# Kernel optimization log

Hardware: AMD Instinct MI355X
Metric: run time of the kernel (lower is better)

## Reference

```python
import jax, jax.numpy as jnp
import numpy as np

N = 43
H = N // 2  # 21


def _mk(key, i, o):
    kw, kb = jax.random.split(key)
    bound = 1.0 / np.sqrt(i)
    W = jax.random.uniform(kw, (i, o), jnp.float32, -bound, bound)
    b = jax.random.uniform(kb, (o,), jnp.float32, -bound, bound)
    return W, b


def setup_inputs() -> dict:
    key = jax.random.key(0)
    keys = jax.random.split(key, 11)
    x = jax.random.normal(keys[0], (1048576, N), jnp.float32)
    dims = [(N, N), (N, N), (N, N), (N, N), (N, H),  # encoder
            (H, N), (N, N), (N, N), (N, N), (N, N)]  # decoder
    out = {"x": x}
    for li, (i, o) in enumerate(dims):
        W, b = _mk(keys[li + 1], i, o)
        out[f"W{li}"] = W
        out[f"b{li}"] = b
    return out


def reference(x, W0, b0, W1, b1, W2, b2, W3, b3, W4, b4,
              W5, b5, W6, b6, W7, b7, W8, b8, W9, b9):
    Ws = [W0, W1, W2, W3, W4, W5, W6, W7, W8, W9]
    bs = [b0, b1, b2, b3, b4, b5, b6, b7, b8, b9]
    h = x
    for li in range(10):
        h = h @ Ws[li] + bs[li]
        # tanh after every layer except encoder bottleneck (4) and final (9)
        if li not in (4, 9):
            h = jnp.tanh(h)
    return h
```

## Files before the change

kernel.cpp:

```cpp
#include <hip/hip_runtime.h>


typedef _Float16 f16x8 __attribute__((ext_vector_type(8)));
typedef float f32x4 __attribute__((ext_vector_type(4)));

#define TPB 512
#define NBLK 256
#define ITERS 16
#define NROWS 1048576
#define NCOL 43
#define WSTRIDE 72
#define WSLOT (48 * WSTRIDE)
#define W_BYTES (10 * WSLOT * 2)
#define XBUF_BYTES 6144
#define X_BASE W_BYTES
#define HBUF_BYTES (32 * WSTRIDE * 2)
#define H_BASE (X_BASE + 8 * XBUF_BYTES)
#define SMEM_BYTES (H_BASE + 8 * HBUF_BYTES)

__device__ __forceinline__ float fast_tanh(float x) {
  float t = __builtin_amdgcn_exp2f(x * 2.8853900817779268f);
  float r = __builtin_amdgcn_rcpf(t + 1.0f);
  return __builtin_fmaf(-2.0f, r, 1.0f);
}

__device__ __forceinline__ void gload_lds16(const void* g, void* l) {
  __builtin_amdgcn_global_load_lds(
      (const __attribute__((address_space(1))) void*)g,
      (__attribute__((address_space(3))) void*)l, 16, 0, 0);
}

__device__ __forceinline__ void issue_dma(const float* x, const char* xlim,
                                          float* xb, size_t rowbase, int lane) {
  const char* base = (const char*)x + rowbase * (size_t)(NCOL * 4);
#pragma unroll
  for (int c = 0; c < 6; ++c) {
    const char* src = base + c * 1024 + lane * 16;
    src = (src > xlim) ? xlim : src;
    gload_lds16(src, (char*)xb + c * 1024);
  }
}

__device__ __forceinline__ void store_h4(_Float16* dst, float v0, float v1,
                                         float v2, float v3) {
  union { _Float16 h[4]; uint2 u; } p;
  p.h[0] = (_Float16)v0; p.h[1] = (_Float16)v1;
  p.h[2] = (_Float16)v2; p.h[3] = (_Float16)v3;
  *(uint2*)dst = p.u;
}

template <int NT, int KC, bool DOTANH, int NLOUT>
__device__ __forceinline__ void mid_layer(const _Float16* __restrict__ Wl,
                                          _Float16* Hw, int g, int lr) {
  f16x8 Bv[2][KC];
#pragma unroll
  for (int s = 0; s < 2; ++s)
#pragma unroll
    for (int c = 0; c < KC; ++c)
      Bv[s][c] = *(const f16x8*)(Hw + (16 * s + lr) * WSTRIDE + 8 * g + 32 * c);

  f32x4 acc[NT][2];
#pragma unroll
  for (int t = 0; t < NT; ++t)
#pragma unroll
    for (int s = 0; s < 2; ++s) acc[t][s] = f32x4{0.f, 0.f, 0.f, 0.f};

#pragma unroll
  for (int c = 0; c < KC; ++c)
#pragma unroll
    for (int t = 0; t < NT; ++t) {
      f16x8 A = *(const f16x8*)(Wl + (16 * t + lr) * WSTRIDE + 8 * g + 32 * c);
#pragma unroll
      for (int s = 0; s < 2; ++s)
        acc[t][s] = __builtin_amdgcn_mfma_f32_16x16x32_f16(A, Bv[s][c],
                                                           acc[t][s], 0, 0, 0);
    }

#pragma unroll
  for (int t = 0; t < NT; ++t)
#pragma unroll
    for (int s = 0; s < 2; ++s) {
      float v[4];
#pragma unroll
      for (int r = 0; r < 4; ++r) {
        int col = 16 * t + 4 * g + r;
        float u = acc[t][s][r];
        if (DOTANH) u = fast_tanh(u);
        v[r] = (col < NLOUT) ? u : ((col == NLOUT) ? 1.0f : 0.0f);
      }
      store_h4(Hw + (16 * s + lr) * WSTRIDE + 16 * t + 4 * g,
               v[0], v[1], v[2], v[3]);
    }
}

extern "C" __global__ void __launch_bounds__(TPB, 2)
ae_kernel(const float* __restrict__ x,
          const float* __restrict__ W0, const float* __restrict__ B0,
          const float* __restrict__ W1, const float* __restrict__ B1,
          const float* __restrict__ W2, const float* __restrict__ B2,
          const float* __restrict__ W3, const float* __restrict__ B3,
          const float* __restrict__ W4, const float* __restrict__ B4,
          const float* __restrict__ W5, const float* __restrict__ B5,
          const float* __restrict__ W6, const float* __restrict__ B6,
          const float* __restrict__ W7, const float* __restrict__ B7,
          const float* __restrict__ W8, const float* __restrict__ B8,
          const float* __restrict__ W9, const float* __restrict__ B9,
          float* __restrict__ out) {
  extern __shared__ char smem[];
  _Float16* lw = (_Float16*)smem;

  const int tid = threadIdx.x;
  const int wave = tid >> 6;
  const int lane = tid & 63;
  const int g = lane >> 4;
  const int lr = lane & 15;

  {
    const float* Wp[10] = {W0, W1, W2, W3, W4, W5, W6, W7, W8, W9};
    const float* Bp[10] = {B0, B1, B2, B3, B4, B5, B6, B7, B8, B9};
    const int KLs[10] = {43, 43, 43, 43, 43, 21, 43, 43, 43, 43};
    const int NLs[10] = {43, 43, 43, 43, 21, 43, 43, 43, 43, 43};
#pragma unroll
    for (int L = 0; L < 10; ++L) {
      const float* Wl = Wp[L];
      const float* Bl = Bp[L];
      const int KL = KLs[L], NL = NLs[L];
      for (int idx = tid; idx < 48 * 64; idx += TPB) {
        int n = idx >> 6, k = idx & 63;
        float v = 0.0f;
        if (n < NL) {
          if (k < KL) v = Wl[k * NL + n];
          else if (k == KL && L != 0) v = Bl[n];
        }
        lw[L * WSLOT + n * WSTRIDE + k] = (_Float16)v;
      }
    }
  }

  float* xb = (float*)(smem + X_BASE + wave * XBUF_BYTES);
  _Float16* Hw = (_Float16*)(smem + H_BASE + wave * HBUF_BYTES);

  {
    unsigned* h32 = (unsigned*)Hw;
#pragma unroll
    for (int i = 0; i < 18; ++i) h32[lane + 64 * i] = 0;
  }

  float b0v[12];
#pragma unroll
  for (int t = 0; t < 3; ++t)
#pragma unroll
    for (int r = 0; r < 4; ++r) {
      int n = 16 * t + 4 * g + r;
      b0v[t * 4 + r] = (n < NCOL) ? B0[n] : 0.0f;
    }

  __syncthreads();

  const char* xlim = (const char*)x + (size_t)NROWS * NCOL * 4 - 16;
  const size_t blockrow = (size_t)blockIdx.x * (ITERS * 256);

  issue_dma(x, xlim, xb, blockrow + (size_t)(wave * 32), lane);

#pragma unroll 1
  for (int it = 0; it < ITERS; ++it) {
    const size_t row0 = blockrow + (size_t)it * 256 + (size_t)(wave * 32);
    asm volatile("s_waitcnt vmcnt(0)" ::: "memory");

    f16x8 Bv[2][2];
#pragma unroll
    for (int s = 0; s < 2; ++s)
#pragma unroll
      for (int c = 0; c < 2; ++c) {
        const float* xr = xb + (16 * s + lr) * NCOL + 8 * g + 32 * c;
        f16x8 v;
#pragma unroll
        for (int j = 0; j < 8; ++j) v[j] = (_Float16)xr[j];
        Bv[s][c] = v;
      }
    asm volatile("s_waitcnt lgkmcnt(0)" ::: "memory");
    if (it < ITERS - 1)
      issue_dma(x, xlim, xb, row0 + 256, lane);

    f32x4 acc[3][2];
#pragma unroll
    for (int t = 0; t < 3; ++t)
#pragma unroll
      for (int s = 0; s < 2; ++s) acc[t][s] = f32x4{0.f, 0.f, 0.f, 0.f};
#pragma unroll
    for (int c = 0; c < 2; ++c)
#pragma unroll
      for (int t = 0; t < 3; ++t) {
        f16x8 A = *(const f16x8*)(lw + (16 * t + lr) * WSTRIDE + 8 * g + 32 * c);
#pragma unroll
        for (int s = 0; s < 2; ++s)
          acc[t][s] = __builtin_amdgcn_mfma_f32_16x16x32_f16(A, Bv[s][c],
                                                             acc[t][s], 0, 0, 0);
      }
#pragma unroll
    for (int t = 0; t < 3; ++t)
#pragma unroll
      for (int s = 0; s < 2; ++s) {
        float v[4];
#pragma unroll
        for (int r = 0; r < 4; ++r) {
          int col = 16 * t + 4 * g + r;
          float u = fast_tanh(acc[t][s][r] + b0v[t * 4 + r]);
          v[r] = (col < NCOL) ? u : ((col == NCOL) ? 1.0f : 0.0f);
        }
        store_h4(Hw + (16 * s + lr) * WSTRIDE + 16 * t + 4 * g,
                 v[0], v[1], v[2], v[3]);
      }

    mid_layer<3, 2, true, 43>(lw + 1 * WSLOT, Hw, g, lr);
    mid_layer<3, 2, true, 43>(lw + 2 * WSLOT, Hw, g, lr);
    mid_layer<3, 2, true, 43>(lw + 3 * WSLOT, Hw, g, lr);
    mid_layer<2, 2, false, 21>(lw + 4 * WSLOT, Hw, g, lr);
    mid_layer<3, 1, true, 43>(lw + 5 * WSLOT, Hw, g, lr);
    mid_layer<3, 2, true, 43>(lw + 6 * WSLOT, Hw, g, lr);
    mid_layer<3, 2, true, 43>(lw + 7 * WSLOT, Hw, g, lr);
    mid_layer<3, 2, true, 43>(lw + 8 * WSLOT, Hw, g, lr);

    {
      f16x8 B9[2][2];
#pragma unroll
      for (int s = 0; s < 2; ++s)
#pragma unroll
        for (int c = 0; c < 2; ++c)
          B9[s][c] = *(const f16x8*)(Hw + (16 * s + lr) * WSTRIDE + 8 * g + 32 * c);
      f32x4 a9[3][2];
#pragma unroll
      for (int t = 0; t < 3; ++t)
#pragma unroll
        for (int s = 0; s < 2; ++s) a9[t][s] = f32x4{0.f, 0.f, 0.f, 0.f};
#pragma unroll
      for (int c = 0; c < 2; ++c)
#pragma unroll
        for (int t = 0; t < 3; ++t) {
          f16x8 A = *(const f16x8*)(lw + 9 * WSLOT + (16 * t + lr) * WSTRIDE +
                                    8 * g + 32 * c);
#pragma unroll
          for (int s = 0; s < 2; ++s)
            a9[t][s] = __builtin_amdgcn_mfma_f32_16x16x32_f16(A, B9[s][c],
                                                              a9[t][s], 0, 0, 0);
        }
#pragma unroll
      for (int t = 0; t < 3; ++t)
#pragma unroll
        for (int s = 0; s < 2; ++s)
#pragma unroll
          for (int r = 0; r < 4; ++r) {
            int col = 16 * t + 4 * g + r;
            if (col < NCOL)
              out[(row0 + (size_t)(16 * s + lr)) * NCOL + col] = a9[t][s][r];
          }
    }
  }
}

extern "C" void kernel_launch(void* const* d_in, const int* in_sizes, int n_in,
                              void* d_out, int out_size, void* d_ws,
                              size_t ws_size, hipStream_t stream) {
  const float* x = (const float*)d_in[0];
  const float* W[10];
  const float* B[10];
  for (int i = 0; i < 10; ++i) {
    W[i] = (const float*)d_in[1 + 2 * i];
    B[i] = (const float*)d_in[2 + 2 * i];
  }
  hipFuncSetAttribute(reinterpret_cast<const void*>(ae_kernel),
                      hipFuncAttributeMaxDynamicSharedMemorySize, SMEM_BYTES);
  ae_kernel<<<dim3(NBLK), dim3(TPB), SMEM_BYTES, stream>>>(
      x, W[0], B[0], W[1], B[1], W[2], B[2], W[3], B[3], W[4], B[4],
      W[5], B[5], W[6], B[6], W[7], B[7], W[8], B[8], W[9], B[9],
      (float*)d_out);
}
```

Before: 169.0 us.

## Load x directly into registers with prefetch, drop LDS DMA staging, double block size

Removes the global-to-LDS DMA staging buffer for the input rows. Each lane now reads its x values straight into registers and prefetches the next iteration's rows during compute. Out-of-range columns are masked with a packed multiply. The block grows to 1024 threads (16 waves) with half the iterations, and conversions to half precision use packed round-toward-zero instructions. This cuts LDS traffic and wait barriers, but the scalar 4-byte global loads are uncoalesced, register pressure goes up, and the kernel is limited to one block per CU.

```diff
diff --git a/kernel.cpp b/kernel.cpp
--- a/kernel.cpp
+++ b/kernel.cpp
@@ -1,22 +1,24 @@
 #include <hip/hip_runtime.h>
 
 
+typedef __fp16 pk16x2 __attribute__((ext_vector_type(2)));
 typedef _Float16 f16x8 __attribute__((ext_vector_type(8)));
 typedef float f32x4 __attribute__((ext_vector_type(4)));
 
-#define TPB 512
+#define TPB 1024
 #define NBLK 256
-#define ITERS 16
+#define ITERS 8
 #define NROWS 1048576
 #define NCOL 43
+#define ROWB 172u
+#define XBYTES (NROWS * (size_t)ROWB)
 #define WSTRIDE 72
 #define WSLOT (48 * WSTRIDE)
 #define W_BYTES (10 * WSLOT * 2)
-#define XBUF_BYTES 6144
-#define X_BASE W_BYTES
-#define HBUF_BYTES (32 * WSTRIDE * 2)
-#define H_BASE (X_BASE + 8 * XBUF_BYTES)
-#define SMEM_BYTES (H_BASE + 8 * HBUF_BYTES)
+#define HBUF_HW (32 * WSTRIDE)
+#define HBUF_BYTES (HBUF_HW * 2)
+#define H_BASE W_BYTES
+#define SMEM_BYTES (H_BASE + 16 * HBUF_BYTES)
 
 __device__ __forceinline__ float fast_tanh(float x) {
   float t = __builtin_amdgcn_exp2f(x * 2.8853900817779268f);
@@ -24,28 +26,11 @@
   return __builtin_fmaf(-2.0f, r, 1.0f);
 }
 
-__device__ __forceinline__ void gload_lds16(const void* g, void* l) {
-  __builtin_amdgcn_global_load_lds(
-      (const __attribute__((address_space(1))) void*)g,
-      (__attribute__((address_space(3))) void*)l, 16, 0, 0);
-}
-
-__device__ __forceinline__ void issue_dma(const float* x, const char* xlim,
-                                          float* xb, size_t rowbase, int lane) {
-  const char* base = (const char*)x + rowbase * (size_t)(NCOL * 4);
-#pragma unroll
-  for (int c = 0; c < 6; ++c) {
-    const char* src = base + c * 1024 + lane * 16;
-    src = (src > xlim) ? xlim : src;
-    gload_lds16(src, (char*)xb + c * 1024);
-  }
-}
-
 __device__ __forceinline__ void store_h4(_Float16* dst, float v0, float v1,
                                          float v2, float v3) {
-  union { _Float16 h[4]; uint2 u; } p;
-  p.h[0] = (_Float16)v0; p.h[1] = (_Float16)v1;
-  p.h[2] = (_Float16)v2; p.h[3] = (_Float16)v3;
+  union { pk16x2 h[2]; uint2 u; } p;
+  p.h[0] = __builtin_amdgcn_cvt_pkrtz(v0, v1);
+  p.h[1] = __builtin_amdgcn_cvt_pkrtz(v2, v3);
   *(uint2*)dst = p.u;
 }
 
@@ -93,7 +78,7 @@
     }
 }
 
-extern "C" __global__ void __launch_bounds__(TPB, 2)
+extern "C" __global__ void __launch_bounds__(TPB, 1)
 ae_kernel(const float* __restrict__ x,
           const float* __restrict__ W0, const float* __restrict__ B0,
           const float* __restrict__ W1, const float* __restrict__ B1,
@@ -137,7 +122,6 @@
     }
   }
 
-  float* xb = (float*)(smem + X_BASE + wave * XBUF_BYTES);
   _Float16* Hw = (_Float16*)(smem + H_BASE + wave * HBUF_BYTES);
 
   {
@@ -155,32 +139,65 @@
       b0v[t * 4 + r] = (n < NCOL) ? B0[n] : 0.0f;
     }
 
+  pk16x2 m1[4];
+#pragma unroll
+  for (int j2 = 0; j2 < 4; ++j2) {
+    m1[j2][0] = (__fp16)((32 + 8 * g + 2 * j2 + 0 < NCOL) ? 1.0f : 0.0f);
+    m1[j2][1] = (__fp16)((32 + 8 * g + 2 * j2 + 1 < NCOL) ? 1.0f : 0.0f);
+  }
+
   __syncthreads();
 
-  const char* xlim = (const char*)x + (size_t)NROWS * NCOL * 4 - 16;
-  const size_t blockrow = (size_t)blockIdx.x * (ITERS * 256);
-
-  issue_dma(x, xlim, xb, blockrow + (size_t)(wave * 32), lane);
+  const char* xc = (const char*)x;
+  const unsigned blockbase = (unsigned)blockIdx.x * (ITERS * 512) + wave * 32;
+  const unsigned LIM = (unsigned)(XBYTES - 4);
+
+  float xv0[2][8], xv1[2][8];
+#pragma unroll
+  for (int s = 0; s < 2; ++s) {
+    unsigned rb = (blockbase + 16 * s + lr) * ROWB;
+    unsigned a0 = rb + 32u * g;
+    unsigned a1 = rb + 128u + 32u * g;
+#pragma unroll
+    for (int j = 0; j < 8; ++j) {
+      xv0[s][j] = *(const float*)(xc + (a0 + 4u * j));
+      unsigned a = a1 + 4u * j;
+      xv1[s][j] = *(const float*)(xc + (a < LIM ? a : LIM));
+    }
+  }
 
 #pragma unroll 1
   for (int it = 0; it < ITERS; ++it) {
-    const size_t row0 = blockrow + (size_t)it * 256 + (size_t)(wave * 32);
-    asm volatile("s_waitcnt vmcnt(0)" ::: "memory");
+    const unsigned row0 = blockbase + (unsigned)it * 512u;
 
     f16x8 Bv[2][2];
 #pragma unroll
-    for (int s = 0; s < 2; ++s)
-#pragma unroll
-      for (int c = 0; c < 2; ++c) {
-        const float* xr = xb + (16 * s + lr) * NCOL + 8 * g + 32 * c;
-        f16x8 v;
-#pragma unroll
-        for (int j = 0; j < 8; ++j) v[j] = (_Float16)xr[j];
-        Bv[s][c] = v;
-      }
-    asm volatile("s_waitcnt lgkmcnt(0)" ::: "memory");
-    if (it < ITERS - 1)
-      issue_dma(x, xlim, xb, row0 + 256, lane);
+    for (int s = 0; s < 2; ++s) {
+      union { pk16x2 h[4]; f16x8 v; } u0, u1;
+#pragma unroll
+      for (int j2 = 0; j2 < 4; ++j2) {
+        u0.h[j2] = __builtin_amdgcn_cvt_pkrtz(xv0[s][2 * j2], xv0[s][2 * j2 + 1]);
+        u1.h[j2] = __builtin_amdgcn_cvt_pkrtz(xv1[s][2 * j2], xv1[s][2 * j2 + 1])
+                   * m1[j2];
+      }
+      Bv[s][0] = u0.v;
+      Bv[s][1] = u1.v;
+    }
+
+    if (it + 1 < ITERS) {
+#pragma unroll
+      for (int s = 0; s < 2; ++s) {
+        unsigned rb = (row0 + 512u + 16 * s + lr) * ROWB;
+        unsigned a0 = rb + 32u * g;
+        unsigned a1 = rb + 128u + 32u * g;
+#pragma unroll
+        for (int j = 0; j < 8; ++j) {
+          xv0[s][j] = *(const float*)(xc + (a0 + 4u * j));
+          unsigned a = a1 + 4u * j;
+          xv1[s][j] = *(const float*)(xc + (a < LIM ? a : LIM));
+        }
+      }
+    }
 
     f32x4 acc[3][2];
 #pragma unroll
@@ -252,7 +269,7 @@
           for (int r = 0; r < 4; ++r) {
             int col = 16 * t + 4 * g + r;
             if (col < NCOL)
-              out[(row0 + (size_t)(16 * s + lr)) * NCOL + col] = a9[t][s][r];
+              out[(size_t)(row0 + 16 * s + lr) * NCOL + col] = a9[t][s][r];
           }
     }
   }
@@ -268,8 +285,9 @@
     W[i] = (const float*)d_in[1 + 2 * i];
     B[i] = (const float*)d_in[2 + 2 * i];
   }
-  hipFuncSetAttribute(reinterpret_cast<const void*>(ae_kernel),
-                      hipFuncAttributeMaxDynamicSharedMemorySize, SMEM_BYTES);
+  (void)hipFuncSetAttribute(reinterpret_cast<const void*>(ae_kernel),
+                            hipFuncAttributeMaxDynamicSharedMemorySize,
+                            SMEM_BYTES);
   ae_kernel<<<dim3(NBLK), dim3(TPB), SMEM_BYTES, stream>>>(
       x, W[0], B[0], W[1], B[1], W[2], B[2], W[3], B[3], W[4], B[4],
       W[5], B[5], W[6], B[6], W[7], B[7], W[8], B[8], W[9], B[9],
```

New measurement: 159.9 us. 5.4% less time.
